# Performance work log

Hardware: AMD Instinct MI355X
Metric: run time of the kernel (lower is better)

The kernel has to match this reference:

```python
import jax, jax.numpy as jnp
import numpy as np

STEPSZ = 0.1
ALPHA = 0.01
BETA = 0.005
FLTRSTDEV = 2.0
NSTEPS = 50
DMAX = 15.0
EXTGRADFAC = 10.0


def make_gauss_edge_fltr(stdev):
    # Separable Gaussian-derivative edge filters, one per spatial dim: [2,1,k,k]
    r = int(np.ceil(3 * stdev))
    xs = np.arange(-r, r + 1, dtype=np.float32)
    g = np.exp(-xs ** 2 / (2 * stdev ** 2)).astype(np.float32)
    g /= g.sum()
    dg = (-xs / (stdev ** 2)) * g
    fy = dg[:, None] * g[None, :]
    fx = g[:, None] * dg[None, :]
    return np.stack([fy, fx])[:, None]  # [2,1,k,k]


def cmpt_grad_im(x, fltr):
    # x: [B,1,H,W] -> [B,2,H,W] spatial gradient image
    return jax.lax.conv_general_dilated(x, fltr, (1, 1), 'SAME',
                                        dimension_numbers=('NCHW', 'OIHW', 'NCHW'))


def bilinear(img, pts):
    # img: [C,H,W], pts: [N,2] (y,x) -> [N,C]
    H, W = img.shape[1], img.shape[2]
    y = jnp.clip(pts[:, 0], 0.0, H - 1.001)
    x = jnp.clip(pts[:, 1], 0.0, W - 1.001)
    y0 = jnp.floor(y).astype(jnp.int32)
    x0 = jnp.floor(x).astype(jnp.int32)
    ty = y - y0
    tx = x - x0
    v00 = img[:, y0, x0]
    v01 = img[:, y0, x0 + 1]
    v10 = img[:, y0 + 1, x0]
    v11 = img[:, y0 + 1, x0 + 1]
    out = v00 * (1 - ty) * (1 - tx) + v01 * (1 - ty) * tx + v10 * ty * (1 - tx) + v11 * ty * tx
    return out.T


def _d2(p):
    # chain second derivative with replicate ends
    return jnp.concatenate([p[:1], p[:-1]]) - 2 * p + jnp.concatenate([p[1:], p[-1:]])


def snake_optim(pos, w, gimg, gimgW, H, W):
    hi = jnp.array([H - 1.0, W - 1.0], dtype=pos.dtype)

    def step(carry, _):
        p, wd = carry
        f = bilinear(gimg, p)                     # external force [N,2]
        d2 = _d2(p)
        d4 = _d2(_d2(p))
        p = jnp.clip(p + STEPSZ * (ALPHA * d2 - BETA * d4 + f), 0.0, hi)
        fw = bilinear(gimgW, p).sum(-1)           # width force [N]
        wd = jnp.clip(wd + STEPSZ * (ALPHA * _d2(wd) + fw), 0.0, DMAX)
        return (p, wd), None

    (pos, w), _ = jax.lax.scan(step, (pos, w), None, length=NSTEPS)
    return pos, w


def render_dmap(pos, w, H, W):
    # distance map with widths: min_n (||pixel - node_n|| - width_n), clipped to [0, dmax]
    yy, xx = jnp.meshgrid(jnp.arange(H, dtype=jnp.float32),
                          jnp.arange(W, dtype=jnp.float32), indexing='ij')
    grid = jnp.stack([yy.ravel(), xx.ravel()], -1)            # [HW,2]
    d = jnp.linalg.norm(grid[:, None, :] - pos[None, :, :], axis=-1) - w[None, :]  # [HW,N]
    return jnp.clip(d.min(axis=1), 0.0, DMAX).reshape(H, W)


def setup_inputs() -> dict:
    key = jax.random.key(0)
    k1, k2, k3 = jax.random.split(key, 3)
    B, H, W, N = 4, 256, 256, 256
    pred_dmap = jax.random.normal(k1, (B, 1, H, W), dtype=jnp.float32)
    node_pos = jax.random.uniform(k2, (B, N, 2), dtype=jnp.float32) * (H - 1)
    widths = jax.random.uniform(k3, (B, N), dtype=jnp.float32) * 3.0
    return {"pred_dmap": pred_dmap, "node_pos": node_pos, "widths": widths}


def reference(pred_dmap, node_pos, widths):
    B, _, H, W = pred_dmap.shape
    fltr = jnp.asarray(make_gauss_edge_fltr(FLTRSTDEV))
    pd = jax.lax.stop_gradient(pred_dmap)          # original detaches before grad-image
    gimg = cmpt_grad_im(pd, fltr) * EXTGRADFAC     # [B,2,H,W]
    gimgW = cmpt_grad_im(jnp.abs(pd), fltr) * EXTGRADFAC

    def per_sample(pos, w, gi, gw):
        p, wd = snake_optim(pos, w, gi, gw, H, W)
        return render_dmap(p, wd, H, W)

    snake_dm = jax.vmap(per_sample)(node_pos, widths, gimg, gimgW)  # [B,H,W]
    snake_dm = jax.lax.stop_gradient(snake_dm)[:, None]             # rendered target, no grad
    return ((pred_dmap - snake_dm) ** 2).mean()
```

## Files before the change

kernel.cpp:

```cpp
#include <hip/hip_runtime.h>
#include <hip/hip_fp16.h>
#include <math.h>

#define HH 256
#define WW 256
#define NB 4
#define NN 256
#define NSTEPS 50
#define STEPSZ 0.1f
#define ALPHA 0.01f
#define BETA 0.005f
#define DMAX 15.0f
#define CTILE 4
#define CH (CTILE + 12)

struct Flt { float g[13]; float dg[13]; };

__global__ void conv_fused_kernel(const float* __restrict__ pd,
                                  uint2* __restrict__ imgH, Flt flt) {
    int blk = blockIdx.x;
    int b = blk >> 6;
    int t = blk & 63;
    int y0 = t * CTILE;
    int x = threadIdx.x;
    __shared__ float srow[CH][WW + 16];
    for (int r = 0; r < CH; ++r) {
        int yy = y0 - 6 + r;
        float v = (yy >= 0 && yy < HH) ? pd[((size_t)b * HH + yy) * WW + x] : 0.f;
        srow[r][6 + x] = v;
        if (x < 6) { srow[r][x] = 0.f; srow[r][WW + 6 + x] = 0.f; }
    }
    __syncthreads();
    float4 h[CH];
#pragma unroll
    for (int r = 0; r < CH; ++r) {
        float sg = 0.f, sdg = 0.f, sga = 0.f, sdga = 0.f;
#pragma unroll
        for (int j = 0; j < 13; ++j) {
            float v = srow[r][x + j];
            float a = fabsf(v);
            sg   += flt.g[j]  * v;
            sdg  += flt.dg[j] * v;
            sga  += flt.g[j]  * a;
            sdga += flt.dg[j] * a;
        }
        h[r] = make_float4(sg, sdg, sga, sdga);
    }
#pragma unroll
    for (int rr = 0; rr < CTILE; ++rr) {
        float g0 = 0.f, g1 = 0.f, w0 = 0.f, w1 = 0.f;
#pragma unroll
        for (int i2 = 0; i2 < 13; ++i2) {
            float4 v = h[rr + i2];
            g0 += flt.dg[i2] * v.x;
            g1 += flt.g[i2]  * v.y;
            w0 += flt.dg[i2] * v.z;
            w1 += flt.g[i2]  * v.w;
        }
        union { uint2 u; __half hh[4]; } o;
        o.hh[0] = __float2half(10.f * g0);
        o.hh[1] = __float2half(10.f * g1);
        o.hh[2] = __float2half(10.f * (w0 + w1));
        o.hh[3] = __float2half(0.f);
        imgH[((size_t)b * HH + y0 + rr) * WW + x] = o.u;
    }
}

__device__ __forceinline__ void sampleH(const uint2* __restrict__ img,
                                        float py_, float px_,
                                        float& fy, float& fx, float& fw) {
    float yc = fminf(fmaxf(py_, 0.f), 254.999f);
    float xc = fminf(fmaxf(px_, 0.f), 254.999f);
    int y0 = (int)yc, x0 = (int)xc;
    float ty = yc - (float)y0, tx = xc - (float)x0;
    const uint2* p = img + y0 * WW + x0;
    union { uint4 u; __half h[8]; } r0, r1;
    r0.u = *(const uint4*)p;
    r1.u = *(const uint4*)(p + WW);
    float w00 = (1.f - ty) * (1.f - tx), w01 = (1.f - ty) * tx;
    float w10 = ty * (1.f - tx),         w11 = ty * tx;
    fy = __half2float(r0.h[0]) * w00 + __half2float(r0.h[4]) * w01 +
         __half2float(r1.h[0]) * w10 + __half2float(r1.h[4]) * w11;
    fx = __half2float(r0.h[1]) * w00 + __half2float(r0.h[5]) * w01 +
         __half2float(r1.h[1]) * w10 + __half2float(r1.h[5]) * w11;
    fw = __half2float(r0.h[2]) * w00 + __half2float(r0.h[6]) * w01 +
         __half2float(r1.h[2]) * w10 + __half2float(r1.h[6]) * w11;
}

__global__ void snake_kernel(const uint2* __restrict__ imgH,
                             const float* __restrict__ node_pos,
                             const float* __restrict__ widths,
                             float4* __restrict__ nodes_out,
                             unsigned* __restrict__ cnt) {
    int b = blockIdx.x;
    int i = threadIdx.x;
    if (b == 0 && i == 0) *cnt = 0;
    __shared__ float2 pbuf[2][NN];
    __shared__ float  wbuf[2][NN];
    const uint2* img = imgH + (size_t)b * HH * WW;
    const float2* np2 = (const float2*)(node_pos + (size_t)b * NN * 2);
    float2 pc = np2[i];
    float wc = widths[(size_t)b * NN + i];
    pbuf[0][i] = pc;
    wbuf[0][i] = wc;
    int im1 = (i > 0) ? i - 1 : 0;
    int im2 = (i > 1) ? i - 2 : 0;
    int ip1 = (i < NN - 1) ? i + 1 : NN - 1;
    int ip2 = (i < NN - 2) ? i + 2 : NN - 1;
    float fy, fx, fw;
    sampleH(img, pc.x, pc.y, fy, fx, fw);
    __syncthreads();
    int cur = 0;
    for (int s = 0; s < NSTEPS; ++s) {
        int nxt = cur ^ 1;
        float wm1 = wbuf[cur][im1], wp1 = wbuf[cur][ip1];
        float d2w = wm1 - 2.f * wc + wp1;
        if (s) wc = fminf(fmaxf(wc + STEPSZ * (ALPHA * d2w + fw), 0.f), DMAX);
        wbuf[nxt][i] = wc;
        float2 pm2 = pbuf[cur][im2], pm1 = pbuf[cur][im1];
        float2 pp1 = pbuf[cur][ip1], pp2 = pbuf[cur][ip2];
        float d2y = pm1.x - 2.f * pc.x + pp1.x;
        float d2x = pm1.y - 2.f * pc.y + pp1.y;
        float d2my = pm2.x - 2.f * pm1.x + pc.x;
        float d2mx = pm2.y - 2.f * pm1.y + pc.y;
        float d2py = pc.x - 2.f * pp1.x + pp2.x;
        float d2px = pc.y - 2.f * pp1.y + pp2.y;
        if (i == 0)      { d2my = d2y; d2mx = d2x; }
        if (i == NN - 1) { d2py = d2y; d2px = d2x; }
        float d4y = d2my - 2.f * d2y + d2py;
        float d4x = d2mx - 2.f * d2x + d2px;
        pc.x = fminf(fmaxf(pc.x + STEPSZ * (ALPHA * d2y - BETA * d4y + fy), 0.f),
                     (float)(HH - 1));
        pc.y = fminf(fmaxf(pc.y + STEPSZ * (ALPHA * d2x - BETA * d4x + fx), 0.f),
                     (float)(WW - 1));
        pbuf[nxt][i] = pc;
        sampleH(img, pc.x, pc.y, fy, fx, fw);
        cur = nxt;
        __syncthreads();
    }
    float wm1 = wbuf[cur][im1], wp1 = wbuf[cur][ip1];
    float d2w = wm1 - 2.f * wc + wp1;
    wc = fminf(fmaxf(wc + STEPSZ * (ALPHA * d2w + fw), 0.f), DMAX);
    nodes_out[(size_t)b * NN + i] = make_float4(pc.x, pc.y, wc, 0.f);
}

__global__ void render_loss_kernel(const float* __restrict__ pd,
                                   const float4* __restrict__ nodes,
                                   float* __restrict__ partial,
                                   unsigned* __restrict__ cnt,
                                   float* __restrict__ out) {
    int blk = blockIdx.x;
    int b = blk >> 8;
    int tile = blk & 255;
    int tx0 = (tile & 7) << 5;
    int ty0 = (tile >> 3) << 3;
    int t = threadIdx.x;
    int lx = t & 31, ly = t >> 5;
    __shared__ float4 list[NN];
    __shared__ int wbase[4];
    __shared__ int total;
    __shared__ float wsum[4];
    __shared__ int lastflag;

    float4 nv = nodes[(size_t)b * NN + t];
    float ddx = fmaxf(fabsf(nv.y - ((float)tx0 + 15.5f)) - 15.5f, 0.f);
    float ddy = fmaxf(fabsf(nv.x - ((float)ty0 + 3.5f)) - 3.5f, 0.f);
    float rad = DMAX + nv.z;
    bool cand = (ddx * ddx + ddy * ddy) < rad * rad;
    unsigned long long mask = __ballot(cand);
    int wid = t >> 6;
    if ((t & 63) == 0) wbase[wid] = __popcll(mask);
    __syncthreads();
    if (t == 0) {
        int s = 0;
#pragma unroll
        for (int wv = 0; wv < 4; ++wv) { int c = wbase[wv]; wbase[wv] = s; s += c; }
        total = s;
    }
    __syncthreads();
    if (cand) {
        int pos = wbase[wid] + __popcll(mask & ((1ULL << (t & 63)) - 1ULL));
        list[pos] = nv;
    }
    __syncthreads();

    float fyc = (float)(ty0 + ly), fxc = (float)(tx0 + lx);
    float v = DMAX;
    int tot = total;
    for (int j = 0; j < tot; ++j) {
        float4 p = list[j];
        float dy = fyc - p.x;
        float dx = fxc - p.y;
        float r2 = dy * dy + dx * dx;
        float tt = v + p.z;
        if (tt > 0.f && r2 < tt * tt)
            v = sqrtf(r2) - p.z;
    }
    float dm = fmaxf(v, 0.f);
    float diff = pd[((size_t)b * HH + ty0 + ly) * WW + tx0 + lx] - dm;
    float val = diff * diff;
    for (int off = 32; off > 0; off >>= 1) val += __shfl_down(val, off, 64);
    if ((t & 63) == 0) wsum[wid] = val;
    __syncthreads();
    if (t == 0) {
        float s = wsum[0] + wsum[1] + wsum[2] + wsum[3];
        __hip_atomic_store(&partial[blk], s, __ATOMIC_RELEASE,
                           __HIP_MEMORY_SCOPE_AGENT);
        unsigned c = __hip_atomic_fetch_add(cnt, 1u, __ATOMIC_ACQ_REL,
                                            __HIP_MEMORY_SCOPE_AGENT);
        lastflag = (c == (unsigned)(NB * 256 - 1));
    }
    __syncthreads();
    if (lastflag) {
        float v2 = 0.f;
        for (int j = t; j < NB * 256; j += 256)
            v2 += __hip_atomic_load(&partial[j], __ATOMIC_ACQUIRE,
                                    __HIP_MEMORY_SCOPE_AGENT);
        for (int off = 32; off > 0; off >>= 1) v2 += __shfl_down(v2, off, 64);
        if ((t & 63) == 0) wsum[wid] = v2;
        __syncthreads();
        if (t == 0)
            out[0] = (wsum[0] + wsum[1] + wsum[2] + wsum[3]) *
                     (1.f / (float)(NB * HH * WW));
    }
}

extern "C" void kernel_launch(void* const* d_in, const int* in_sizes, int n_in,
                              void* d_out, int out_size, void* d_ws, size_t ws_size,
                              hipStream_t stream) {
    const float* pd       = (const float*)d_in[0];
    const float* node_pos = (const float*)d_in[1];
    const float* widths   = (const float*)d_in[2];
    float* out = (float*)d_out;

    char* ws = (char*)d_ws;
    size_t img_bytes = (size_t)NB * HH * WW * sizeof(uint2);
    uint2*    imgH    = (uint2*)ws;
    float4*   nodes   = (float4*)(ws + img_bytes);
    float*    partial = (float*)(ws + img_bytes + (size_t)NB * NN * sizeof(float4));
    unsigned* cnt     = (unsigned*)(partial + NB * 256);

    Flt flt;
    {
        float g[13];
        float s = 0.f;
        for (int i = 0; i < 13; ++i) {
            float xx = (float)(i - 6);
            g[i] = expf(-xx * xx / 8.f);
            s += g[i];
        }
        for (int i = 0; i < 13; ++i) {
            flt.g[i]  = g[i] / s;
            flt.dg[i] = -(float)(i - 6) / 4.f * flt.g[i];
        }
    }

    conv_fused_kernel<<<NB * 64, 256, 0, stream>>>(pd, imgH, flt);
    snake_kernel<<<NB, NN, 0, stream>>>(imgH, node_pos, widths, nodes, cnt);
    render_loss_kernel<<<NB * 256, 256, 0, stream>>>(pd, nodes, partial, cnt, out);
}
```

Before: 127.5 us.

## Store pre-gathered 2x2 bilinear cells per pixel and merge snake shared buffers

The conv kernel now computes one extra halo row and writes, for each pixel, a 32-byte record holding all 12 half-precision values of its 2x2 bilinear neighbourhood. Each sample in the serial snake loop then needs a single contiguous read instead of two loads from separate rows. The snake kernel also packs position and width into one float4 shared buffer and moves the width update after the next sample is issued, so that work can overlap the gather latency. The cost is a fourfold larger intermediate image written by the conv kernel, plus an extra shared staging array and sync there.

```diff
diff --git a/kernel.cpp b/kernel.cpp
--- a/kernel.cpp
+++ b/kernel.cpp
@@ -12,18 +12,19 @@
 #define BETA 0.005f
 #define DMAX 15.0f
 #define CTILE 4
-#define CH (CTILE + 12)
+#define CH (CTILE + 1 + 12)
 
 struct Flt { float g[13]; float dg[13]; };
 
 __global__ void conv_fused_kernel(const float* __restrict__ pd,
-                                  uint2* __restrict__ imgH, Flt flt) {
+                                  uint4* __restrict__ rec, Flt flt) {
     int blk = blockIdx.x;
     int b = blk >> 6;
     int t = blk & 63;
     int y0 = t * CTILE;
     int x = threadIdx.x;
     __shared__ float srow[CH][WW + 16];
+    __shared__ float vres[CTILE + 1][WW + 2][3];
     for (int r = 0; r < CH; ++r) {
         int yy = y0 - 6 + r;
         float v = (yy >= 0 && yy < HH) ? pd[((size_t)b * HH + yy) * WW + x] : 0.f;
@@ -47,7 +48,7 @@
         h[r] = make_float4(sg, sdg, sga, sdga);
     }
 #pragma unroll
-    for (int rr = 0; rr < CTILE; ++rr) {
+    for (int rr = 0; rr <= CTILE; ++rr) {
         float g0 = 0.f, g1 = 0.f, w0 = 0.f, w1 = 0.f;
 #pragma unroll
         for (int i2 = 0; i2 < 13; ++i2) {
@@ -57,37 +58,56 @@
             w0 += flt.dg[i2] * v.z;
             w1 += flt.g[i2]  * v.w;
         }
-        union { uint2 u; __half hh[4]; } o;
-        o.hh[0] = __float2half(10.f * g0);
-        o.hh[1] = __float2half(10.f * g1);
-        o.hh[2] = __float2half(10.f * (w0 + w1));
-        o.hh[3] = __float2half(0.f);
-        imgH[((size_t)b * HH + y0 + rr) * WW + x] = o.u;
-    }
-}
-
-__device__ __forceinline__ void sampleH(const uint2* __restrict__ img,
+        vres[rr][x][0] = 10.f * g0;
+        vres[rr][x][1] = 10.f * g1;
+        vres[rr][x][2] = 10.f * (w0 + w1);
+    }
+    __syncthreads();
+#pragma unroll
+    for (int rr = 0; rr < CTILE; ++rr) {
+        const float* c00 = vres[rr][x];
+        const float* c01 = vres[rr][x + 1];
+        const float* c10 = vres[rr + 1][x];
+        const float* c11 = vres[rr + 1][x + 1];
+        union { uint4 u; __half hh[8]; } lo;
+        union { uint2 u; __half hh[4]; } hi;
+        lo.hh[0] = __float2half(c00[0]); lo.hh[1] = __float2half(c00[1]);
+        lo.hh[2] = __float2half(c00[2]);
+        lo.hh[3] = __float2half(c01[0]); lo.hh[4] = __float2half(c01[1]);
+        lo.hh[5] = __float2half(c01[2]);
+        lo.hh[6] = __float2half(c10[0]); lo.hh[7] = __float2half(c10[1]);
+        hi.hh[0] = __float2half(c10[2]);
+        hi.hh[1] = __float2half(c11[0]); hi.hh[2] = __float2half(c11[1]);
+        hi.hh[3] = __float2half(c11[2]);
+        size_t ridx = ((size_t)b * HH + y0 + rr) * WW + x;
+        rec[ridx * 2] = lo.u;
+        *((uint2*)(rec + ridx * 2 + 1)) = hi.u;
+    }
+}
+
+__device__ __forceinline__ void sampleR(const uint4* __restrict__ rec,
                                         float py_, float px_,
                                         float& fy, float& fx, float& fw) {
     float yc = fminf(fmaxf(py_, 0.f), 254.999f);
     float xc = fminf(fmaxf(px_, 0.f), 254.999f);
     int y0 = (int)yc, x0 = (int)xc;
     float ty = yc - (float)y0, tx = xc - (float)x0;
-    const uint2* p = img + y0 * WW + x0;
-    union { uint4 u; __half h[8]; } r0, r1;
-    r0.u = *(const uint4*)p;
-    r1.u = *(const uint4*)(p + WW);
+    const uint4* p = rec + (size_t)((y0 << 8) + x0) * 2;
+    union { uint4 u; __half h[8]; } lo;
+    union { uint2 u; __half h[4]; } hi;
+    lo.u = p[0];
+    hi.u = *(const uint2*)(p + 1);
     float w00 = (1.f - ty) * (1.f - tx), w01 = (1.f - ty) * tx;
     float w10 = ty * (1.f - tx),         w11 = ty * tx;
-    fy = __half2float(r0.h[0]) * w00 + __half2float(r0.h[4]) * w01 +
-         __half2float(r1.h[0]) * w10 + __half2float(r1.h[4]) * w11;
-    fx = __half2float(r0.h[1]) * w00 + __half2float(r0.h[5]) * w01 +
-         __half2float(r1.h[1]) * w10 + __half2float(r1.h[5]) * w11;
-    fw = __half2float(r0.h[2]) * w00 + __half2float(r0.h[6]) * w01 +
-         __half2float(r1.h[2]) * w10 + __half2float(r1.h[6]) * w11;
-}
-
-__global__ void snake_kernel(const uint2* __restrict__ imgH,
+    fy = __half2float(lo.h[0]) * w00 + __half2float(lo.h[3]) * w01 +
+         __half2float(lo.h[6]) * w10 + __half2float(hi.h[1]) * w11;
+    fx = __half2float(lo.h[1]) * w00 + __half2float(lo.h[4]) * w01 +
+         __half2float(lo.h[7]) * w10 + __half2float(hi.h[2]) * w11;
+    fw = __half2float(lo.h[2]) * w00 + __half2float(lo.h[5]) * w01 +
+         __half2float(hi.h[0]) * w10 + __half2float(hi.h[3]) * w11;
+}
+
+__global__ void snake_kernel(const uint4* __restrict__ rec,
                              const float* __restrict__ node_pos,
                              const float* __restrict__ widths,
                              float4* __restrict__ nodes_out,
@@ -95,36 +115,30 @@
     int b = blockIdx.x;
     int i = threadIdx.x;
     if (b == 0 && i == 0) *cnt = 0;
-    __shared__ float2 pbuf[2][NN];
-    __shared__ float  wbuf[2][NN];
-    const uint2* img = imgH + (size_t)b * HH * WW;
+    __shared__ float4 buf[2][NN];
+    const uint4* img = rec + (size_t)b * HH * WW * 2;
     const float2* np2 = (const float2*)(node_pos + (size_t)b * NN * 2);
     float2 pc = np2[i];
     float wc = widths[(size_t)b * NN + i];
-    pbuf[0][i] = pc;
-    wbuf[0][i] = wc;
+    buf[0][i] = make_float4(pc.x, pc.y, wc, 0.f);
     int im1 = (i > 0) ? i - 1 : 0;
     int im2 = (i > 1) ? i - 2 : 0;
     int ip1 = (i < NN - 1) ? i + 1 : NN - 1;
     int ip2 = (i < NN - 2) ? i + 2 : NN - 1;
     float fy, fx, fw;
-    sampleH(img, pc.x, pc.y, fy, fx, fw);
+    sampleR(img, pc.x, pc.y, fy, fx, fw);
     __syncthreads();
     int cur = 0;
     for (int s = 0; s < NSTEPS; ++s) {
         int nxt = cur ^ 1;
-        float wm1 = wbuf[cur][im1], wp1 = wbuf[cur][ip1];
-        float d2w = wm1 - 2.f * wc + wp1;
-        if (s) wc = fminf(fmaxf(wc + STEPSZ * (ALPHA * d2w + fw), 0.f), DMAX);
-        wbuf[nxt][i] = wc;
-        float2 pm2 = pbuf[cur][im2], pm1 = pbuf[cur][im1];
-        float2 pp1 = pbuf[cur][ip1], pp2 = pbuf[cur][ip2];
-        float d2y = pm1.x - 2.f * pc.x + pp1.x;
-        float d2x = pm1.y - 2.f * pc.y + pp1.y;
-        float d2my = pm2.x - 2.f * pm1.x + pc.x;
-        float d2mx = pm2.y - 2.f * pm1.y + pc.y;
-        float d2py = pc.x - 2.f * pp1.x + pp2.x;
-        float d2px = pc.y - 2.f * pp1.y + pp2.y;
+        float4 m2 = buf[cur][im2], m1 = buf[cur][im1];
+        float4 p1 = buf[cur][ip1], p2 = buf[cur][ip2];
+        float d2y = m1.x - 2.f * pc.x + p1.x;
+        float d2x = m1.y - 2.f * pc.y + p1.y;
+        float d2my = m2.x - 2.f * m1.x + pc.x;
+        float d2mx = m2.y - 2.f * m1.y + pc.y;
+        float d2py = pc.x - 2.f * p1.x + p2.x;
+        float d2px = pc.y - 2.f * p1.y + p2.y;
         if (i == 0)      { d2my = d2y; d2mx = d2x; }
         if (i == NN - 1) { d2py = d2y; d2px = d2x; }
         float d4y = d2my - 2.f * d2y + d2py;
@@ -133,12 +147,17 @@
                      (float)(HH - 1));
         pc.y = fminf(fmaxf(pc.y + STEPSZ * (ALPHA * d2x - BETA * d4x + fx), 0.f),
                      (float)(WW - 1));
-        pbuf[nxt][i] = pc;
-        sampleH(img, pc.x, pc.y, fy, fx, fw);
+        *((float2*)&buf[nxt][i]) = pc;
+        float nfy, nfx, nfw;
+        sampleR(img, pc.x, pc.y, nfy, nfx, nfw);
+        float d2w = m1.z - 2.f * wc + p1.z;
+        if (s) wc = fminf(fmaxf(wc + STEPSZ * (ALPHA * d2w + fw), 0.f), DMAX);
+        buf[nxt][i].z = wc;
+        fy = nfy; fx = nfx; fw = nfw;
         cur = nxt;
         __syncthreads();
     }
-    float wm1 = wbuf[cur][im1], wp1 = wbuf[cur][ip1];
+    float wm1 = buf[cur][im1].z, wp1 = buf[cur][ip1].z;
     float d2w = wm1 - 2.f * wc + wp1;
     wc = fminf(fmaxf(wc + STEPSZ * (ALPHA * d2w + fw), 0.f), DMAX);
     nodes_out[(size_t)b * NN + i] = make_float4(pc.x, pc.y, wc, 0.f);
@@ -234,10 +253,10 @@
     float* out = (float*)d_out;
 
     char* ws = (char*)d_ws;
-    size_t img_bytes = (size_t)NB * HH * WW * sizeof(uint2);
-    uint2*    imgH    = (uint2*)ws;
-    float4*   nodes   = (float4*)(ws + img_bytes);
-    float*    partial = (float*)(ws + img_bytes + (size_t)NB * NN * sizeof(float4));
+    size_t rec_bytes = (size_t)NB * HH * WW * 32;
+    uint4*    rec     = (uint4*)ws;
+    float4*   nodes   = (float4*)(ws + rec_bytes);
+    float*    partial = (float*)(ws + rec_bytes + (size_t)NB * NN * sizeof(float4));
     unsigned* cnt     = (unsigned*)(partial + NB * 256);
 
     Flt flt;
@@ -255,7 +274,7 @@
         }
     }
 
-    conv_fused_kernel<<<NB * 64, 256, 0, stream>>>(pd, imgH, flt);
-    snake_kernel<<<NB, NN, 0, stream>>>(imgH, node_pos, widths, nodes, cnt);
+    conv_fused_kernel<<<NB * 64, 256, 0, stream>>>(pd, rec, flt);
+    snake_kernel<<<NB, NN, 0, stream>>>(rec, node_pos, widths, nodes, cnt);
     render_loss_kernel<<<NB * 256, 256, 0, stream>>>(pd, nodes, partial, cnt, out);
 }
```

Result: no change. 125.8 us, median of 2 (-1.3%).
